# Optimization experiments

Measured on AMD Instinct MI355X. Metric: run time of the kernel, lower is better.

## Reference

```python
import jax, jax.numpy as jnp
import numpy as np

B, C, N, K, OUT = 4, 192, 10000, 16, 384

def setup_inputs() -> dict:
    key = jax.random.key(0)
    k1, k2, k3, k4 = jax.random.split(key, 4)
    x = jax.random.normal(k1, (B, C, N, 1), dtype=jnp.float32)
    edge_index = jax.random.randint(k2, (2, B, N, K), 0, N, dtype=jnp.int32)
    # 1x1x1 Conv3d weight [OUT, 2C, 1, 1, 1] collapsed to [OUT, 2C]
    fan_in = 2 * C
    weight = jax.random.normal(k3, (OUT, 2 * C), dtype=jnp.float32) / np.sqrt(fan_in)
    bias = jax.random.normal(k4, (OUT,), dtype=jnp.float32) * 0.01
    return {"x": x, "edge_index": edge_index, "weight": weight, "bias": bias}


def _gather_neighbors(x3, idx):
    # x3: [B, C, N], idx: [B, N, K] -> [B, C, N, K]
    return jax.vmap(lambda xb, ib: xb[:, ib])(x3, idx)


def reference(x, edge_index, weight, bias):
    b, c, n, _ = x.shape
    x3 = x[..., 0]                                   # [B, C, N]
    x_i = _gather_neighbors(x3, edge_index[1])       # centers  [B, C, N, K]
    x_j = _gather_neighbors(x3, edge_index[0])       # neighbors [B, C, N, K]
    x_j_max = jnp.max(x_j - x_i, axis=-1)            # max-relative, [B, C, N]
    # torch.cat([x.unsqueeze(2), x_j.unsqueeze(2)], 2).reshape(b, 2c, n, 1)
    # interleaves channels as (x_c, xj_c) pairs
    feat = jnp.stack([x3, x_j_max], axis=2).reshape(b, 2 * c, n)  # [B, 2C, N]
    out = jnp.einsum('oc,bcn->bon', weight, feat) + bias[None, :, None]
    out = jax.nn.relu(out)
    # Conv3d path: output shape [B, OUT, N, 1, 1]
    return out[..., None, None]
```

## Files before the change

kernel.cpp:

```cpp
#include <hip/hip_runtime.h>


#define NB   4
#define NC   192
#define NN   10000
#define NK   16
#define NOUT 384
#define K2C  384

typedef short bf16x8 __attribute__((ext_vector_type(8)));
typedef float f32x4  __attribute__((ext_vector_type(4)));

__device__ inline unsigned short f2bf(float f) {
    unsigned int u = __builtin_bit_cast(unsigned int, f);
    u += ((u >> 16) & 1u) + 0x7FFFu;
    return (unsigned short)(u >> 16);
}
__device__ inline float bflo(unsigned int u) {
    return __builtin_bit_cast(float, u << 16);
}
__device__ inline float bfhi(unsigned int u) {
    return __builtin_bit_cast(float, u & 0xFFFF0000u);
}

__global__ __launch_bounds__(256) void k_prep(const float* __restrict__ x,
                                              unsigned short* __restrict__ xT,
                                              const float* __restrict__ w,
                                              unsigned short* __restrict__ wbf) {
    __shared__ unsigned short tile[NC * 65];
    int bid = blockIdx.x;
    if (bid >= 628) {
        int i = (bid - 628) * 256 + threadIdx.x;
        float4 v = ((const float4*)w)[i];
        uint2 o;
        o.x = (unsigned int)f2bf(v.x) | ((unsigned int)f2bf(v.y) << 16);
        o.y = (unsigned int)f2bf(v.z) | ((unsigned int)f2bf(v.w) << 16);
        ((uint2*)wbf)[i] = o;
        return;
    }
    int b  = bid & 3;
    int nb = (bid >> 2) * 64;
    int t  = threadIdx.x;
    const float* xb = x + (size_t)b * NC * NN;
    for (int i = 0; i < 48; ++i) {
        int idx = i * 256 + t;
        int c  = idx >> 6;
        int nl = idx & 63;
        int n  = nb + nl;
        float v = (n < NN) ? xb[(size_t)c * NN + n] : 0.f;
        tile[c * 65 + nl] = f2bf(v);
    }
    __syncthreads();
    unsigned short* xTb = xT + (size_t)b * NN * NC;
    for (int i = 0; i < 48; ++i) {
        int idx = i * 256 + t;
        int nl  = idx / NC;
        int c   = idx - nl * NC;
        int n   = nb + nl;
        if (n < NN) xTb[(size_t)n * NC + c] = tile[c * 65 + nl];
    }
}

__global__ __launch_bounds__(256, 3) void k_fused(const unsigned short* __restrict__ xT,
                                                  const int* __restrict__ eidx,
                                                  const unsigned short* __restrict__ wbf,
                                                  const float* __restrict__ bias,
                                                  float* __restrict__ out) {
    __shared__ unsigned short lds[64 * 48 * 8];
    int bid  = blockIdx.x;
    int b    = bid & 3;
    int nt   = bid >> 2;
    int wv   = threadIdx.x >> 6;
    int lane = threadIdx.x & 63;
    int lam  = lane & 31;
    int hb   = lane & 32;
    int r    = lane & 15;
    int q    = lane >> 4;

    const unsigned int* xr = (const unsigned int*)(xT + (size_t)b * NN * NC);
    int part = lam >> 4;
    const int* ep = eidx + (size_t)part * NB * NN * NK + (size_t)b * NN * NK;
    int nlb = wv * 16 + (hb ? 8 : 0);
    int gnb = nt * 64 + nlb;

    int v[8];
#pragma unroll
    for (int it = 0; it < 8; ++it) {
        int n = gnb + it;
        v[it] = (n < NN) ? ep[(size_t)n * NK + (lam & 15)] : 0;
    }

    uint2* l2 = (uint2*)lds;
    for (int it = 0; it < 8; ++it) {
        int n = gnb + it;
        if (n >= NN) break;
        int nl = nlb + it;
        const unsigned int* crow = xr + (size_t)n * 96;
        unsigned int c0 = crow[lam], c1 = crow[32 + lam], c2 = crow[64 + lam];
        float m0l = -INFINITY, m0h = -INFINITY;
        float m1l = -INFINITY, m1h = -INFINITY;
        float m2l = -INFINITY, m2h = -INFINITY;
#pragma unroll 4
        for (int k = 0; k < 16; ++k) {
            int j = __shfl(v[it], hb + k, 64);
            int i = __shfl(v[it], hb + 16 + k, 64);
            const unsigned int* rj = xr + (size_t)j * 96;
            const unsigned int* ri = xr + (size_t)i * 96;
            unsigned int j0 = rj[lam], j1 = rj[32 + lam], j2 = rj[64 + lam];
            unsigned int i0 = ri[lam], i1 = ri[32 + lam], i2 = ri[64 + lam];
            m0l = fmaxf(m0l, bflo(j0) - bflo(i0));  m0h = fmaxf(m0h, bfhi(j0) - bfhi(i0));
            m1l = fmaxf(m1l, bflo(j1) - bflo(i1));  m1h = fmaxf(m1h, bfhi(j1) - bfhi(i1));
            m2l = fmaxf(m2l, bflo(j2) - bflo(i2));  m2h = fmaxf(m2h, bfhi(j2) - bfhi(i2));
        }
        uint2 o0, o1, o2;
        o0.x = (c0 & 0xFFFFu)  | ((unsigned int)f2bf(m0l) << 16);
        o0.y = (c0 >> 16)      | ((unsigned int)f2bf(m0h) << 16);
        o1.x = (c1 & 0xFFFFu)  | ((unsigned int)f2bf(m1l) << 16);
        o1.y = (c1 >> 16)      | ((unsigned int)f2bf(m1h) << 16);
        o2.x = (c2 & 0xFFFFu)  | ((unsigned int)f2bf(m2l) << 16);
        o2.y = (c2 >> 16)      | ((unsigned int)f2bf(m2h) << 16);
        unsigned int g  = (unsigned int)(lam >> 1);
        unsigned int nw = (unsigned int)nl;
        unsigned int s0 = nw * 48u + (g        + 3u * nw) % 48u;
        unsigned int s1 = nw * 48u + (g + 16u  + 3u * nw) % 48u;
        unsigned int s2 = nw * 48u + (g + 32u  + 3u * nw) % 48u;
        unsigned int half = (unsigned int)(lam & 1);
        l2[2u * s0 + half] = o0;
        l2[2u * s1 + half] = o1;
        l2[2u * s2 + half] = o2;
    }

    __syncthreads();

    const unsigned short* aptr = wbf + (size_t)(wv * 96 + r) * K2C + q * 8;

    unsigned int nbase[4], u0[4];
#pragma unroll
    for (int ni = 0; ni < 4; ++ni) {
        unsigned int n = ni * 16 + r;
        nbase[ni] = n * 48u;
        u0[ni] = ((unsigned int)q + 3u * n) % 48u;
    }

    f32x4 acc[6][4];
#pragma unroll
    for (int mi = 0; mi < 6; ++mi)
#pragma unroll
        for (int ni = 0; ni < 4; ++ni)
            acc[mi][ni] = (f32x4){0.f, 0.f, 0.f, 0.f};

#pragma unroll 2
    for (int t = 0; t < 12; ++t) {
        bf16x8 a[6], bb[4];
#pragma unroll
        for (int mi = 0; mi < 6; ++mi)
            a[mi] = *(const bf16x8*)(aptr + (size_t)mi * 16 * K2C + t * 32);
#pragma unroll
        for (int ni = 0; ni < 4; ++ni) {
            unsigned int u = u0[ni] + 4u * t;
            if (u >= 48u) u -= 48u;
            bb[ni] = *(const bf16x8*)(lds + (size_t)(nbase[ni] + u) * 8);
        }
#pragma unroll
        for (int mi = 0; mi < 6; ++mi)
#pragma unroll
            for (int ni = 0; ni < 4; ++ni)
                acc[mi][ni] = __builtin_amdgcn_mfma_f32_16x16x32_bf16(a[mi], bb[ni], acc[mi][ni], 0, 0, 0);
    }

    float* ob = out + (size_t)b * NOUT * NN;
#pragma unroll
    for (int mi = 0; mi < 6; ++mi) {
        int obase = wv * 96 + mi * 16 + q * 4;
#pragma unroll
        for (int ni = 0; ni < 4; ++ni) {
            int n = nt * 64 + ni * 16 + r;
            if (n < NN) {
#pragma unroll
                for (int rr = 0; rr < 4; ++rr) {
                    int o = obase + rr;
                    float val = acc[mi][ni][rr] + bias[o];
                    ob[(size_t)o * NN + n] = fmaxf(val, 0.f);
                }
            }
        }
    }
}

extern "C" void kernel_launch(void* const* d_in, const int* in_sizes, int n_in,
                              void* d_out, int out_size, void* d_ws, size_t ws_size,
                              hipStream_t stream) {
    const float* x    = (const float*)d_in[0];
    const int*   eidx = (const int*)d_in[1];
    const float* w    = (const float*)d_in[2];
    const float* bias = (const float*)d_in[3];
    float* out = (float*)d_out;

    unsigned short* xT  = (unsigned short*)d_ws;
    unsigned short* wbf = xT + (size_t)NB * NN * NC;

    hipLaunchKernelGGL(k_prep,  dim3(628 + 144), dim3(256), 0, stream, x, xT, w, wbf);
    hipLaunchKernelGGL(k_fused, dim3(4 * 157),   dim3(256), 0, stream, xT, eidx, wbf, bias, out);
}
```

Before: 167.3 us.

## Vectorize neighbor gather to 16-byte loads with software-pipelined batches

Each half-wave now reads a neighbor row as 24 uint4 loads per lane instead of three scalar 32-bit loads per lane, so each lane handles 8 channels. The 16 neighbor loads are split into four batches of four, double-buffered so the next batch loads while the previous one is reduced. The LDS store moves to 16-byte writes. Eight of the 32 lanes in each half-wave now sit idle on loads and stores, and occupancy drops from 3 to 2 blocks per CU to make room for the extra registers.

Result: slower. 181.9 us (+8.7%).

```diff
diff --git a/kernel.cpp b/kernel.cpp
--- a/kernel.cpp
+++ b/kernel.cpp
@@ -61,7 +61,34 @@
     }
 }
 
-__global__ __launch_bounds__(256, 3) void k_fused(const unsigned short* __restrict__ xT,
+#define LOADG(JA, IA, KB)                                         \
+    {                                                             \
+        _Pragma("unroll")                                         \
+        for (int kk = 0; kk < 4; ++kk) {                          \
+            int j = __shfl(v[it], hb + (KB) + kk, 64);            \
+            int i = __shfl(v[it], hb + 16 + (KB) + kk, 64);       \
+            JA[kk] = xr4[(size_t)j * 24 + le];                    \
+            IA[kk] = xr4[(size_t)i * 24 + le];                    \
+        }                                                         \
+    }
+
+#define CONSG(JA, IA)                                             \
+    {                                                             \
+        _Pragma("unroll")                                         \
+        for (int kk = 0; kk < 4; ++kk) {                          \
+            uint4 jv = JA[kk], iv = IA[kk];                       \
+            m0 = fmaxf(m0, bflo(jv.x) - bflo(iv.x));              \
+            m1 = fmaxf(m1, bfhi(jv.x) - bfhi(iv.x));              \
+            m2 = fmaxf(m2, bflo(jv.y) - bflo(iv.y));              \
+            m3 = fmaxf(m3, bfhi(jv.y) - bfhi(iv.y));              \
+            m4 = fmaxf(m4, bflo(jv.z) - bflo(iv.z));              \
+            m5 = fmaxf(m5, bfhi(jv.z) - bfhi(iv.z));              \
+            m6 = fmaxf(m6, bflo(jv.w) - bflo(iv.w));              \
+            m7 = fmaxf(m7, bfhi(jv.w) - bfhi(iv.w));              \
+        }                                                         \
+    }
+
+__global__ __launch_bounds__(256, 2) void k_fused(const unsigned short* __restrict__ xT,
                                                   const int* __restrict__ eidx,
                                                   const unsigned short* __restrict__ wbf,
                                                   const float* __restrict__ bias,
@@ -70,18 +97,21 @@
     int bid  = blockIdx.x;
     int b    = bid & 3;
     int nt   = bid >> 2;
-    int wv   = threadIdx.x >> 6;
-    int lane = threadIdx.x & 63;
-    int lam  = lane & 31;
+    int tid  = threadIdx.x;
+    int wv   = tid >> 6;
+    int lane = tid & 63;
+    int hw   = tid >> 5;
+    int lam  = tid & 31;
     int hb   = lane & 32;
     int r    = lane & 15;
     int q    = lane >> 4;
 
-    const unsigned int* xr = (const unsigned int*)(xT + (size_t)b * NN * NC);
+    const uint4* xr4 = (const uint4*)(xT + (size_t)b * NN * NC);
     int part = lam >> 4;
     const int* ep = eidx + (size_t)part * NB * NN * NK + (size_t)b * NN * NK;
-    int nlb = wv * 16 + (hb ? 8 : 0);
+    int nlb = hw * 8;
     int gnb = nt * 64 + nlb;
+    int le  = (lam < 24) ? lam : 0;
 
     int v[8];
 #pragma unroll
@@ -90,44 +120,41 @@
         v[it] = (n < NN) ? ep[(size_t)n * NK + (lam & 15)] : 0;
     }
 
-    uint2* l2 = (uint2*)lds;
+    uint4* l4 = (uint4*)lds;
     for (int it = 0; it < 8; ++it) {
         int n = gnb + it;
         if (n >= NN) break;
         int nl = nlb + it;
-        const unsigned int* crow = xr + (size_t)n * 96;
-        unsigned int c0 = crow[lam], c1 = crow[32 + lam], c2 = crow[64 + lam];
-        float m0l = -INFINITY, m0h = -INFINITY;
-        float m1l = -INFINITY, m1h = -INFINITY;
-        float m2l = -INFINITY, m2h = -INFINITY;
-#pragma unroll 4
-        for (int k = 0; k < 16; ++k) {
-            int j = __shfl(v[it], hb + k, 64);
-            int i = __shfl(v[it], hb + 16 + k, 64);
-            const unsigned int* rj = xr + (size_t)j * 96;
-            const unsigned int* ri = xr + (size_t)i * 96;
-            unsigned int j0 = rj[lam], j1 = rj[32 + lam], j2 = rj[64 + lam];
-            unsigned int i0 = ri[lam], i1 = ri[32 + lam], i2 = ri[64 + lam];
-            m0l = fmaxf(m0l, bflo(j0) - bflo(i0));  m0h = fmaxf(m0h, bfhi(j0) - bfhi(i0));
-            m1l = fmaxf(m1l, bflo(j1) - bflo(i1));  m1h = fmaxf(m1h, bfhi(j1) - bfhi(i1));
-            m2l = fmaxf(m2l, bflo(j2) - bflo(i2));  m2h = fmaxf(m2h, bfhi(j2) - bfhi(i2));
+        uint4 c4 = xr4[(size_t)n * 24 + le];
+        float m0 = -INFINITY, m1 = -INFINITY, m2 = -INFINITY, m3 = -INFINITY;
+        float m4 = -INFINITY, m5 = -INFINITY, m6 = -INFINITY, m7 = -INFINITY;
+
+        uint4 ja[4], ia[4], jb_[4], ib_[4];
+        LOADG(ja, ia, 0)
+        LOADG(jb_, ib_, 4)
+        CONSG(ja, ia)
+        LOADG(ja, ia, 8)
+        CONSG(jb_, ib_)
+        LOADG(jb_, ib_, 12)
+        CONSG(ja, ia)
+        CONSG(jb_, ib_)
+
+        if (lam < 24) {
+            unsigned int d0 = (c4.x & 0xFFFFu) | ((unsigned int)f2bf(m0) << 16);
+            unsigned int d1 = (c4.x >> 16)     | ((unsigned int)f2bf(m1) << 16);
+            unsigned int d2 = (c4.y & 0xFFFFu) | ((unsigned int)f2bf(m2) << 16);
+            unsigned int d3 = (c4.y >> 16)     | ((unsigned int)f2bf(m3) << 16);
+            unsigned int d4 = (c4.z & 0xFFFFu) | ((unsigned int)f2bf(m4) << 16);
+            unsigned int d5 = (c4.z >> 16)     | ((unsigned int)f2bf(m5) << 16);
+            unsigned int d6 = (c4.w & 0xFFFFu) | ((unsigned int)f2bf(m6) << 16);
+            unsigned int d7 = (c4.w >> 16)     | ((unsigned int)f2bf(m7) << 16);
+            unsigned int nw = (unsigned int)nl;
+            unsigned int g0 = 2u * (unsigned int)lam;
+            unsigned int s0 = nw * 48u + (g0 + 3u * nw) % 48u;
+            unsigned int s1 = nw * 48u + (g0 + 1u + 3u * nw) % 48u;
+            l4[s0] = (uint4){d0, d1, d2, d3};
+            l4[s1] = (uint4){d4, d5, d6, d7};
         }
-        uint2 o0, o1, o2;
-        o0.x = (c0 & 0xFFFFu)  | ((unsigned int)f2bf(m0l) << 16);
-        o0.y = (c0 >> 16)      | ((unsigned int)f2bf(m0h) << 16);
-        o1.x = (c1 & 0xFFFFu)  | ((unsigned int)f2bf(m1l) << 16);
-        o1.y = (c1 >> 16)      | ((unsigned int)f2bf(m1h) << 16);
-        o2.x = (c2 & 0xFFFFu)  | ((unsigned int)f2bf(m2l) << 16);
-        o2.y = (c2 >> 16)      | ((unsigned int)f2bf(m2h) << 16);
-        unsigned int g  = (unsigned int)(lam >> 1);
-        unsigned int nw = (unsigned int)nl;
-        unsigned int s0 = nw * 48u + (g        + 3u * nw) % 48u;
-        unsigned int s1 = nw * 48u + (g + 16u  + 3u * nw) % 48u;
-        unsigned int s2 = nw * 48u + (g + 32u  + 3u * nw) % 48u;
-        unsigned int half = (unsigned int)(lam & 1);
-        l2[2u * s0 + half] = o0;
-        l2[2u * s1 + half] = o1;
-        l2[2u * s2 + half] = o2;
     }
 
     __syncthreads();
```

## Gather one node per wave with scalar index loads and 8-byte row reads

Applied to the files above, without the earlier changes.

Restructures the gather phase so each wave processes one node at a time, with 48 lanes each reading a uint2 (4 bf16 channels) of a neighbor row. Edge indices are now fetched through wave-uniform (readfirstlane) pointers as scalar loads instead of per-lane loads plus shuffles, and 8 neighbor/center row loads are batched before the max reduction to raise memory-level parallelism. Results are written to LDS as 16-byte stores. The occupancy hint drops from 3 to 2 blocks per SIMD to allow more registers for the batched loads, and 16 of 64 lanes sit idle during the gather.

New measurement: 198.2 us. +18.4%, slower.

```diff
diff --git a/kernel.cpp b/kernel.cpp
--- a/kernel.cpp
+++ b/kernel.cpp
@@ -21,6 +21,11 @@
 }
 __device__ inline float bfhi(unsigned int u) {
     return __builtin_bit_cast(float, u & 0xFFFF0000u);
+}
+__device__ inline unsigned long long uq(unsigned long long a) {
+    unsigned int lo = __builtin_amdgcn_readfirstlane((unsigned int)a);
+    unsigned int hi = __builtin_amdgcn_readfirstlane((unsigned int)(a >> 32));
+    return ((unsigned long long)hi << 32) | lo;
 }
 
 __global__ __launch_bounds__(256) void k_prep(const float* __restrict__ x,
@@ -61,7 +66,7 @@
     }
 }
 
-__global__ __launch_bounds__(256, 3) void k_fused(const unsigned short* __restrict__ xT,
+__global__ __launch_bounds__(256, 2) void k_fused(const unsigned short* __restrict__ xT,
                                                   const int* __restrict__ eidx,
                                                   const unsigned short* __restrict__ wbf,
                                                   const float* __restrict__ bias,
@@ -70,64 +75,58 @@
     int bid  = blockIdx.x;
     int b    = bid & 3;
     int nt   = bid >> 2;
-    int wv   = threadIdx.x >> 6;
-    int lane = threadIdx.x & 63;
-    int lam  = lane & 31;
-    int hb   = lane & 32;
+    int tid  = threadIdx.x;
+    int wv   = tid >> 6;
+    int lane = tid & 63;
     int r    = lane & 15;
     int q    = lane >> 4;
-
-    const unsigned int* xr = (const unsigned int*)(xT + (size_t)b * NN * NC);
-    int part = lam >> 4;
-    const int* ep = eidx + (size_t)part * NB * NN * NK + (size_t)b * NN * NK;
-    int nlb = wv * 16 + (hb ? 8 : 0);
-    int gnb = nt * 64 + nlb;
-
-    int v[8];
-#pragma unroll
-    for (int it = 0; it < 8; ++it) {
-        int n = gnb + it;
-        v[it] = (n < NN) ? ep[(size_t)n * NK + (lam & 15)] : 0;
-    }
-
-    uint2* l2 = (uint2*)lds;
-    for (int it = 0; it < 8; ++it) {
+    int le   = (lane < 48) ? lane : (lane - 48);
+
+    const uint2* xr2 = (const uint2*)(xT + (size_t)b * NN * NC);
+    const int* ep0 = eidx + (size_t)b * NN * NK;
+    const int* ep1 = eidx + (size_t)NB * NN * NK + (size_t)b * NN * NK;
+    int gnb = nt * 64 + wv * 16;
+
+    for (int it = 0; it < 16; ++it) {
         int n = gnb + it;
         if (n >= NN) break;
-        int nl = nlb + it;
-        const unsigned int* crow = xr + (size_t)n * 96;
-        unsigned int c0 = crow[lam], c1 = crow[32 + lam], c2 = crow[64 + lam];
-        float m0l = -INFINITY, m0h = -INFINITY;
-        float m1l = -INFINITY, m1h = -INFINITY;
-        float m2l = -INFINITY, m2h = -INFINITY;
-#pragma unroll 4
-        for (int k = 0; k < 16; ++k) {
-            int j = __shfl(v[it], hb + k, 64);
-            int i = __shfl(v[it], hb + 16 + k, 64);
-            const unsigned int* rj = xr + (size_t)j * 96;
-            const unsigned int* ri = xr + (size_t)i * 96;
-            unsigned int j0 = rj[lam], j1 = rj[32 + lam], j2 = rj[64 + lam];
-            unsigned int i0 = ri[lam], i1 = ri[32 + lam], i2 = ri[64 + lam];
-            m0l = fmaxf(m0l, bflo(j0) - bflo(i0));  m0h = fmaxf(m0h, bfhi(j0) - bfhi(i0));
-            m1l = fmaxf(m1l, bflo(j1) - bflo(i1));  m1h = fmaxf(m1h, bfhi(j1) - bfhi(i1));
-            m2l = fmaxf(m2l, bflo(j2) - bflo(i2));  m2h = fmaxf(m2h, bfhi(j2) - bfhi(i2));
-        }
-        uint2 o0, o1, o2;
-        o0.x = (c0 & 0xFFFFu)  | ((unsigned int)f2bf(m0l) << 16);
-        o0.y = (c0 >> 16)      | ((unsigned int)f2bf(m0h) << 16);
-        o1.x = (c1 & 0xFFFFu)  | ((unsigned int)f2bf(m1l) << 16);
-        o1.y = (c1 >> 16)      | ((unsigned int)f2bf(m1h) << 16);
-        o2.x = (c2 & 0xFFFFu)  | ((unsigned int)f2bf(m2l) << 16);
-        o2.y = (c2 >> 16)      | ((unsigned int)f2bf(m2h) << 16);
-        unsigned int g  = (unsigned int)(lam >> 1);
-        unsigned int nw = (unsigned int)nl;
-        unsigned int s0 = nw * 48u + (g        + 3u * nw) % 48u;
-        unsigned int s1 = nw * 48u + (g + 16u  + 3u * nw) % 48u;
-        unsigned int s2 = nw * 48u + (g + 32u  + 3u * nw) % 48u;
-        unsigned int half = (unsigned int)(lam & 1);
-        l2[2u * s0 + half] = o0;
-        l2[2u * s1 + half] = o1;
-        l2[2u * s2 + half] = o2;
+        const int*  pj = (const int*) uq((unsigned long long)(ep0 + (size_t)n * NK));
+        const int*  pi = (const int*) uq((unsigned long long)(ep1 + (size_t)n * NK));
+        const uint2* rc = (const uint2*)uq((unsigned long long)(xr2 + (size_t)n * 48));
+        uint2 cv = rc[le];
+        float m0 = -INFINITY, m1 = -INFINITY, m2 = -INFINITY, m3 = -INFINITY;
+#pragma unroll
+        for (int h = 0; h < 2; ++h) {
+            int js[8], is_[8];
+#pragma unroll
+            for (int k = 0; k < 8; ++k) {
+                js[k]  = pj[h * 8 + k];
+                is_[k] = pi[h * 8 + k];
+            }
+            uint2 jv[8], iv[8];
+#pragma unroll
+            for (int k = 0; k < 8; ++k) {
+                jv[k] = xr2[(size_t)js[k]  * 48 + le];
+                iv[k] = xr2[(size_t)is_[k] * 48 + le];
+            }
+#pragma unroll
+            for (int k = 0; k < 8; ++k) {
+                m0 = fmaxf(m0, bflo(jv[k].x) - bflo(iv[k].x));
+                m1 = fmaxf(m1, bfhi(jv[k].x) - bfhi(iv[k].x));
+                m2 = fmaxf(m2, bflo(jv[k].y) - bflo(iv[k].y));
+                m3 = fmaxf(m3, bfhi(jv[k].y) - bfhi(iv[k].y));
+            }
+        }
+        if (lane < 48) {
+            unsigned int d0 = (cv.x & 0xFFFFu) | ((unsigned int)f2bf(m0) << 16);
+            unsigned int d1 = (cv.x >> 16)     | ((unsigned int)f2bf(m1) << 16);
+            unsigned int d2 = (cv.y & 0xFFFFu) | ((unsigned int)f2bf(m2) << 16);
+            unsigned int d3 = (cv.y >> 16)     | ((unsigned int)f2bf(m3) << 16);
+            unsigned int nw = (unsigned int)(wv * 16 + it);
+            unsigned int s  = nw * 48u + ((unsigned int)le + 3u * nw) % 48u;
+            uint4 o; o.x = d0; o.y = d1; o.z = d2; o.w = d3;
+            ((uint4*)lds)[s] = o;
+        }
     }
 
     __syncthreads();
```
